# Kernel tuning notes

Measured on AMD Instinct MI355X. Metric: run time of the kernel, lower is better.

The kernel has to match this reference:

```python
import jax, jax.numpy as jnp
import numpy as np

B, SQ, SKV, D = 4, 4096, 4096, 64

def setup_inputs() -> dict:
    key = jax.random.key(0)
    kq, kk, kv = jax.random.split(key, 3)
    return {
        "q": jax.random.normal(kq, (B, SQ, D), dtype=jnp.float32),
        "k": jax.random.normal(kk, (B, SKV, D), dtype=jnp.float32),
        "v": jax.random.normal(kv, (B, SKV, D), dtype=jnp.float32),
        "inv_scale_factor": 8,
        "is_training": 0,
    }

def reference(q, k, v, inv_scale_factor, is_training):
    # qk = q @ k^T, divided by inv_scale_factor, softmax over keys
    scores = jnp.einsum("bqd,bkd->bqk", q, k) / inv_scale_factor  # [B,SQ,SKV]
    attn = jax.nn.softmax(scores, axis=-1)
    # dropout is deterministic identity (eval mode, is_training=0)
    out = jnp.einsum("bqk,bkd->bqd", attn, v)  # [B,SQ,D]
    # should_apply_residual before loop
    out = out + q
    # 3-iteration chain: residual add + normalization add (+2q), dropout (identity),
    # sigmoid, clamp(0,1)
    for _ in range(3):
        out = out + 2.0 * q
        out = jax.nn.sigmoid(out)
        out = jnp.clip(out, 0.0, 1.0)
    return out
```

## Files before the change

### kernel.cpp

```cpp
#include <hip/hip_runtime.h>

#define SQd 4096
#define SKVd 4096
#define DDIM 64
#define BQ 64
#define BK 32
#define NGROUP 4
#define NTILES (SKVd / BK)
#define TILES_PER_GROUP (NTILES / NGROUP)
#define FRAG_ELEMS 512
#define TILE_ELEMS (4 * FRAG_ELEMS)
#define KWS_ELEMS (4 * NTILES * TILE_ELEMS)

typedef __bf16 bf16x8 __attribute__((ext_vector_type(8)));
typedef __bf16 bf16x2 __attribute__((ext_vector_type(2)));
typedef float floatx4 __attribute__((ext_vector_type(4)));

struct CombS {
    float Ored[BQ][NGROUP][68];
    float Lred[BQ][NGROUP];
};
constexpr size_t SMEM_BYTES = sizeof(CombS);

__global__ __launch_bounds__(256)
void prepack_kernel(const float* __restrict__ k, const float* __restrict__ v,
                    __bf16* __restrict__ ws)
{
    const int t = blockIdx.x * 256 + threadIdx.x;
    const int id   = t & (KWS_ELEMS / 8 - 1);
    const int lane = id & 63;
    const int l16  = lane & 15;
    const int quad = lane >> 4;
    const int h    = (id >> 6) & 3;
    const int tile = (id >> 8) & (NTILES - 1);
    const int b    = id >> 15;
    bf16x8 o;
    if (t < KWS_ELEMS / 8) {
        const int row = tile * BK + (h >> 1) * 16 + l16;
        const int col = (h & 1) * 32 + quad * 8;
        const float* p = k + ((size_t)b * SKVd + row) * DDIM + col;
        const float4 a0 = *(const float4*)p;
        const float4 a1 = *(const float4*)(p + 4);
        o[0] = (__bf16)a0.x; o[1] = (__bf16)a0.y; o[2] = (__bf16)a0.z; o[3] = (__bf16)a0.w;
        o[4] = (__bf16)a1.x; o[5] = (__bf16)a1.y; o[6] = (__bf16)a1.z; o[7] = (__bf16)a1.w;
        ((bf16x8*)ws)[id] = o;
    } else {
        const int col = h * 16 + l16;
        #pragma unroll
        for (int j = 0; j < 8; ++j) {
            const int kk  = quad * 8 + j;
            const int key = tile * BK + (kk >> 1) + 16 * (kk & 1);
            o[j] = (__bf16)v[((size_t)b * SKVd + key) * DDIM + col];
        }
        ((bf16x8*)(ws + KWS_ELEMS))[id] = o;
    }
}

__global__ __launch_bounds__(1024, 4)
void fattn_kernel(const float* __restrict__ q, const int* __restrict__ isf_p,
                  const __bf16* __restrict__ kws, const __bf16* __restrict__ vws,
                  float* __restrict__ out)
{
    __shared__ __align__(16) char smem_raw[SMEM_BYTES];

    const int tid  = threadIdx.x;
    const int wave = tid >> 6;
    const int lane = tid & 63;
    const int l16  = lane & 15;
    const int quad = lane >> 4;
    const int g    = wave >> 2;
    const int wg   = wave & 3;

    __bf16 (*Pw)[40] = (__bf16(*)[40])(smem_raw + wave * 1280);

    const int bidx  = blockIdx.x;
    const int b     = (bidx & 7) >> 1;
    const int qtile = ((bidx & 1) << 5) | (bidx >> 3);

    const float scale = 1.0f / (float)(*isf_p);

    bf16x8 qf[2];
    {
        const int qrow = qtile * BQ + wg * 16 + l16;
        const float* qp = q + ((size_t)b * SQd + qrow) * DDIM + quad * 8;
        #pragma unroll
        for (int hh = 0; hh < 2; ++hh)
            #pragma unroll
            for (int j = 0; j < 8; ++j)
                qf[hh][j] = (__bf16)(qp[hh * 32 + j] * scale);
    }

    const __bf16* kg = kws + ((size_t)b * NTILES + g * TILES_PER_GROUP) * TILE_ELEMS + lane * 8;
    const __bf16* vg = vws + ((size_t)b * NTILES + g * TILES_PER_GROUP) * TILE_ELEMS + lane * 8;

    floatx4 o[4];
    float l_lane[4];
    #pragma unroll
    for (int r = 0; r < 4; ++r) l_lane[r] = 0.0f;
    #pragma unroll
    for (int nb = 0; nb < 4; ++nb)
        #pragma unroll
        for (int r = 0; r < 4; ++r) o[nb][r] = 0.0f;

    const floatx4 zf = {0.0f, 0.0f, 0.0f, 0.0f};

    bf16x8 kf[2][4], vf[2][4];
    #pragma unroll
    for (int h = 0; h < 4; ++h) {
        kf[0][h] = *(const bf16x8*)(kg + h * FRAG_ELEMS);
        vf[0][h] = *(const bf16x8*)(vg + h * FRAG_ELEMS);
    }

    #pragma unroll 2
    for (int it = 0; it < TILES_PER_GROUP; ++it) {
        const int cur = it & 1;
        const int nxt = cur ^ 1;
        const size_t noff = (size_t)(it + 1 < TILES_PER_GROUP ? it + 1 : it) * TILE_ELEMS;
        #pragma unroll
        for (int h = 0; h < 4; ++h) {
            kf[nxt][h] = *(const bf16x8*)(kg + noff + h * FRAG_ELEMS);
            vf[nxt][h] = *(const bf16x8*)(vg + noff + h * FRAG_ELEMS);
        }

        floatx4 s0 = zf, s1 = zf;
        s0 = __builtin_amdgcn_mfma_f32_16x16x32_bf16(qf[0], kf[cur][0], s0, 0, 0, 0);
        s0 = __builtin_amdgcn_mfma_f32_16x16x32_bf16(qf[1], kf[cur][1], s0, 0, 0, 0);
        s1 = __builtin_amdgcn_mfma_f32_16x16x32_bf16(qf[0], kf[cur][2], s1, 0, 0, 0);
        s1 = __builtin_amdgcn_mfma_f32_16x16x32_bf16(qf[1], kf[cur][3], s1, 0, 0, 0);

        #pragma unroll
        for (int r = 0; r < 4; ++r) {
            const float p0 = __expf(s0[r]);
            const float p1 = __expf(s1[r]);
            l_lane[r] += p0 + p1;
            bf16x2 pp;
            pp[0] = (__bf16)p0;
            pp[1] = (__bf16)p1;
            *(bf16x2*)&Pw[quad * 4 + r][2 * l16] = pp;
        }
        const bf16x8 pf = *(const bf16x8*)&Pw[l16][quad * 8];

        #pragma unroll
        for (int nb = 0; nb < 4; ++nb)
            o[nb] = __builtin_amdgcn_mfma_f32_16x16x32_bf16(pf, vf[cur][nb], o[nb], 0, 0, 0);
    }

    #pragma unroll
    for (int r = 0; r < 4; ++r) {
        l_lane[r] += __shfl_xor(l_lane[r], 1);
        l_lane[r] += __shfl_xor(l_lane[r], 2);
        l_lane[r] += __shfl_xor(l_lane[r], 4);
        l_lane[r] += __shfl_xor(l_lane[r], 8);
    }

    __syncthreads();
    CombS& C = *(CombS*)smem_raw;
    #pragma unroll
    for (int nb = 0; nb < 4; ++nb)
        #pragma unroll
        for (int r = 0; r < 4; ++r)
            C.Ored[wg * 16 + quad * 4 + r][g][nb * 16 + l16] = o[nb][r];
    if (l16 == 0) {
        #pragma unroll
        for (int r = 0; r < 4; ++r)
            C.Lred[wg * 16 + quad * 4 + r][g] = l_lane[r];
    }
    __syncthreads();

    {
        const int row = tid >> 4;
        const int d4  = (tid & 15) * 4;
        const float l = C.Lred[row][0] + C.Lred[row][1] + C.Lred[row][2] + C.Lred[row][3];
        float x0 = 0.f, x1 = 0.f, x2 = 0.f, x3 = 0.f;
        #pragma unroll
        for (int gg = 0; gg < NGROUP; ++gg) {
            const float4 og = *(const float4*)&C.Ored[row][gg][d4];
            x0 += og.x; x1 += og.y; x2 += og.z; x3 += og.w;
        }
        const size_t idx = ((size_t)b * SQd + qtile * BQ + row) * DDIM + d4;
        const float4 q4 = *(const float4*)(q + idx);
        const float rl = 1.0f / l;
        float xs[4] = {x0 * rl + q4.x, x1 * rl + q4.y, x2 * rl + q4.z, x3 * rl + q4.w};
        const float qs[4] = {q4.x, q4.y, q4.z, q4.w};
        #pragma unroll
        for (int c = 0; c < 4; ++c) {
            float x = xs[c];
            #pragma unroll
            for (int itc = 0; itc < 3; ++itc) {
                x = x + 2.0f * qs[c];
                x = 1.0f / (1.0f + __expf(-x));
                x = fminf(fmaxf(x, 0.0f), 1.0f);
            }
            xs[c] = x;
        }
        const float4 r4 = {xs[0], xs[1], xs[2], xs[3]};
        *(float4*)(out + idx) = r4;
    }
}

extern "C" void kernel_launch(void* const* d_in, const int* in_sizes, int n_in,
                              void* d_out, int out_size, void* d_ws, size_t ws_size,
                              hipStream_t stream) {
    const float* q = (const float*)d_in[0];
    const float* k = (const float*)d_in[1];
    const float* v = (const float*)d_in[2];
    const int* isf = (const int*)d_in[3];
    float* out = (float*)d_out;
    __bf16* ws = (__bf16*)d_ws;

    prepack_kernel<<<dim3(1024), dim3(256), 0, stream>>>(k, v, ws);

    const int nblocks = 4 * (SQd / BQ);
    fattn_kernel<<<dim3(nblocks), dim3(1024), 0, stream>>>(
        q, isf, ws, ws + KWS_ELEMS, out);
}
```

Baseline: 105.9 us.

## Have each wave cover all 64 query rows and keep P in registers

Each wave now handles all four 16-row query groups against its own slice of the key/value tiles (8 key groups, 512-thread blocks), so every K/V fragment load is reused four times. QK^T is computed transposed (K as the A operand) so the exp'd scores already sit in the MFMA B-operand layout. This removes the per-tile LDS round trip for P, with the V prepack permuted to match. The cost is much higher register pressure (16 output accumulators and 8 Q fragments per wave) and a two-phase LDS reduction across 8 groups.

```diff
diff --git a/kernel.cpp b/kernel.cpp
--- a/kernel.cpp
+++ b/kernel.cpp
@@ -5,22 +5,20 @@
 #define DDIM 64
 #define BQ 64
 #define BK 32
-#define NGROUP 4
+#define NG 8
 #define NTILES (SKVd / BK)
-#define TILES_PER_GROUP (NTILES / NGROUP)
+#define TPG (NTILES / NG)
 #define FRAG_ELEMS 512
 #define TILE_ELEMS (4 * FRAG_ELEMS)
 #define KWS_ELEMS (4 * NTILES * TILE_ELEMS)
 
 typedef __bf16 bf16x8 __attribute__((ext_vector_type(8)));
-typedef __bf16 bf16x2 __attribute__((ext_vector_type(2)));
 typedef float floatx4 __attribute__((ext_vector_type(4)));
 
 struct CombS {
-    float Ored[BQ][NGROUP][68];
-    float Lred[BQ][NGROUP];
+    float Ored[BQ][4][68];
+    float Lred[BQ][NG];
 };
-constexpr size_t SMEM_BYTES = sizeof(CombS);
 
 __global__ __launch_bounds__(256)
 void prepack_kernel(const float* __restrict__ k, const float* __restrict__ v,
@@ -48,30 +46,25 @@
         const int col = h * 16 + l16;
         #pragma unroll
         for (int j = 0; j < 8; ++j) {
-            const int kk  = quad * 8 + j;
-            const int key = tile * BK + (kk >> 1) + 16 * (kk & 1);
+            const int key = tile * BK + 16 * (j >> 2) + quad * 4 + (j & 3);
             o[j] = (__bf16)v[((size_t)b * SKVd + key) * DDIM + col];
         }
         ((bf16x8*)(ws + KWS_ELEMS))[id] = o;
     }
 }
 
-__global__ __launch_bounds__(1024, 4)
+__global__ __launch_bounds__(512, 2)
 void fattn_kernel(const float* __restrict__ q, const int* __restrict__ isf_p,
                   const __bf16* __restrict__ kws, const __bf16* __restrict__ vws,
                   float* __restrict__ out)
 {
-    __shared__ __align__(16) char smem_raw[SMEM_BYTES];
+    __shared__ __align__(16) CombS C;
 
     const int tid  = threadIdx.x;
-    const int wave = tid >> 6;
+    const int g    = tid >> 6;
     const int lane = tid & 63;
     const int l16  = lane & 15;
     const int quad = lane >> 4;
-    const int g    = wave >> 2;
-    const int wg   = wave & 3;
-
-    __bf16 (*Pw)[40] = (__bf16(*)[40])(smem_raw + wave * 1280);
 
     const int bidx  = blockIdx.x;
     const int b     = (bidx & 7) >> 1;
@@ -79,122 +72,149 @@
 
     const float scale = 1.0f / (float)(*isf_p);
 
-    bf16x8 qf[2];
+    bf16x8 qf[4][2];
+    #pragma unroll
+    for (int qg = 0; qg < 4; ++qg) {
+        const int qrow = qtile * BQ + qg * 16 + l16;
+        const float* qp = q + ((size_t)b * SQd + qrow) * DDIM + quad * 8;
+        #pragma unroll
+        for (int dh = 0; dh < 2; ++dh) {
+            const float4 a0 = *(const float4*)(qp + dh * 32);
+            const float4 a1 = *(const float4*)(qp + dh * 32 + 4);
+            qf[qg][dh][0] = (__bf16)(a0.x * scale); qf[qg][dh][1] = (__bf16)(a0.y * scale);
+            qf[qg][dh][2] = (__bf16)(a0.z * scale); qf[qg][dh][3] = (__bf16)(a0.w * scale);
+            qf[qg][dh][4] = (__bf16)(a1.x * scale); qf[qg][dh][5] = (__bf16)(a1.y * scale);
+            qf[qg][dh][6] = (__bf16)(a1.z * scale); qf[qg][dh][7] = (__bf16)(a1.w * scale);
+        }
+    }
+
+    const __bf16* kg = kws + ((size_t)b * NTILES + g * TPG) * TILE_ELEMS + lane * 8;
+    const __bf16* vg = vws + ((size_t)b * NTILES + g * TPG) * TILE_ELEMS + lane * 8;
+
+    floatx4 o[4][4];
+    float l_acc[4];
+    #pragma unroll
+    for (int qg = 0; qg < 4; ++qg) {
+        l_acc[qg] = 0.0f;
+        #pragma unroll
+        for (int nb = 0; nb < 4; ++nb)
+            #pragma unroll
+            for (int r = 0; r < 4; ++r) o[qg][nb][r] = 0.0f;
+    }
+
+    const floatx4 zf = {0.0f, 0.0f, 0.0f, 0.0f};
+
+    auto step = [&](bf16x8* kc, bf16x8* vc, bf16x8* kn, bf16x8* vn, int itn) {
+        const size_t noff = (size_t)itn * TILE_ELEMS;
+        #pragma unroll
+        for (int h = 0; h < 4; ++h)
+            kn[h] = *(const bf16x8*)(kg + noff + h * FRAG_ELEMS);
+        #pragma unroll
+        for (int h = 0; h < 4; ++h)
+            vn[h] = *(const bf16x8*)(vg + noff + h * FRAG_ELEMS);
+
+        bf16x8 pf[4];
+        #pragma unroll
+        for (int qg = 0; qg < 4; ++qg) {
+            floatx4 s0 = zf, s1 = zf;
+            s0 = __builtin_amdgcn_mfma_f32_16x16x32_bf16(kc[0], qf[qg][0], s0, 0, 0, 0);
+            s0 = __builtin_amdgcn_mfma_f32_16x16x32_bf16(kc[1], qf[qg][1], s0, 0, 0, 0);
+            s1 = __builtin_amdgcn_mfma_f32_16x16x32_bf16(kc[2], qf[qg][0], s1, 0, 0, 0);
+            s1 = __builtin_amdgcn_mfma_f32_16x16x32_bf16(kc[3], qf[qg][1], s1, 0, 0, 0);
+            float lsum = 0.0f;
+            #pragma unroll
+            for (int r = 0; r < 4; ++r) {
+                const float p0 = __expf(s0[r]);
+                const float p1 = __expf(s1[r]);
+                pf[qg][r]     = (__bf16)p0;
+                pf[qg][4 + r] = (__bf16)p1;
+                lsum += p0 + p1;
+            }
+            l_acc[qg] += lsum;
+        }
+        #pragma unroll
+        for (int nb = 0; nb < 4; ++nb)
+            #pragma unroll
+            for (int qg = 0; qg < 4; ++qg)
+                o[qg][nb] = __builtin_amdgcn_mfma_f32_16x16x32_bf16(pf[qg], vc[nb], o[qg][nb], 0, 0, 0);
+    };
+
+    bf16x8 k0[4], v0[4], k1[4], v1[4];
+    #pragma unroll
+    for (int h = 0; h < 4; ++h) {
+        k0[h] = *(const bf16x8*)(kg + h * FRAG_ELEMS);
+        v0[h] = *(const bf16x8*)(vg + h * FRAG_ELEMS);
+    }
+    for (int t = 0; t < TPG / 2; ++t) {
+        step(k0, v0, k1, v1, 2 * t + 1);
+        step(k1, v1, k0, v0, (2 * t + 2 < TPG) ? 2 * t + 2 : TPG - 1);
+    }
+
+    #pragma unroll
+    for (int qg = 0; qg < 4; ++qg) {
+        l_acc[qg] += __shfl_xor(l_acc[qg], 16);
+        l_acc[qg] += __shfl_xor(l_acc[qg], 32);
+    }
+    if (quad == 0) {
+        #pragma unroll
+        for (int qg = 0; qg < 4; ++qg)
+            C.Lred[qg * 16 + l16][g] = l_acc[qg];
+    }
+
+    if (g < 4) {
+        #pragma unroll
+        for (int qg = 0; qg < 4; ++qg)
+            #pragma unroll
+            for (int nb = 0; nb < 4; ++nb)
+                #pragma unroll
+                for (int r = 0; r < 4; ++r)
+                    C.Ored[qg * 16 + quad * 4 + r][g][nb * 16 + l16] = o[qg][nb][r];
+    }
+    __syncthreads();
+    if (g >= 4) {
+        #pragma unroll
+        for (int qg = 0; qg < 4; ++qg)
+            #pragma unroll
+            for (int nb = 0; nb < 4; ++nb)
+                #pragma unroll
+                for (int r = 0; r < 4; ++r)
+                    C.Ored[qg * 16 + quad * 4 + r][g - 4][nb * 16 + l16] += o[qg][nb][r];
+    }
+    __syncthreads();
+
     {
-        const int qrow = qtile * BQ + wg * 16 + l16;
-        const float* qp = q + ((size_t)b * SQd + qrow) * DDIM + quad * 8;
-        #pragma unroll
-        for (int hh = 0; hh < 2; ++hh)
-            #pragma unroll
-            for (int j = 0; j < 8; ++j)
-                qf[hh][j] = (__bf16)(qp[hh * 32 + j] * scale);
-    }
-
-    const __bf16* kg = kws + ((size_t)b * NTILES + g * TILES_PER_GROUP) * TILE_ELEMS + lane * 8;
-    const __bf16* vg = vws + ((size_t)b * NTILES + g * TILES_PER_GROUP) * TILE_ELEMS + lane * 8;
-
-    floatx4 o[4];
-    float l_lane[4];
-    #pragma unroll
-    for (int r = 0; r < 4; ++r) l_lane[r] = 0.0f;
-    #pragma unroll
-    for (int nb = 0; nb < 4; ++nb)
-        #pragma unroll
-        for (int r = 0; r < 4; ++r) o[nb][r] = 0.0f;
-
-    const floatx4 zf = {0.0f, 0.0f, 0.0f, 0.0f};
-
-    bf16x8 kf[2][4], vf[2][4];
-    #pragma unroll
-    for (int h = 0; h < 4; ++h) {
-        kf[0][h] = *(const bf16x8*)(kg + h * FRAG_ELEMS);
-        vf[0][h] = *(const bf16x8*)(vg + h * FRAG_ELEMS);
-    }
-
-    #pragma unroll 2
-    for (int it = 0; it < TILES_PER_GROUP; ++it) {
-        const int cur = it & 1;
-        const int nxt = cur ^ 1;
-        const size_t noff = (size_t)(it + 1 < TILES_PER_GROUP ? it + 1 : it) * TILE_ELEMS;
-        #pragma unroll
-        for (int h = 0; h < 4; ++h) {
-            kf[nxt][h] = *(const bf16x8*)(kg + noff + h * FRAG_ELEMS);
-            vf[nxt][h] = *(const bf16x8*)(vg + noff + h * FRAG_ELEMS);
-        }
-
-        floatx4 s0 = zf, s1 = zf;
-        s0 = __builtin_amdgcn_mfma_f32_16x16x32_bf16(qf[0], kf[cur][0], s0, 0, 0, 0);
-        s0 = __builtin_amdgcn_mfma_f32_16x16x32_bf16(qf[1], kf[cur][1], s0, 0, 0, 0);
-        s1 = __builtin_amdgcn_mfma_f32_16x16x32_bf16(qf[0], kf[cur][2], s1, 0, 0, 0);
-        s1 = __builtin_amdgcn_mfma_f32_16x16x32_bf16(qf[1], kf[cur][3], s1, 0, 0, 0);
-
-        #pragma unroll
-        for (int r = 0; r < 4; ++r) {
-            const float p0 = __expf(s0[r]);
-            const float p1 = __expf(s1[r]);
-            l_lane[r] += p0 + p1;
-            bf16x2 pp;
-            pp[0] = (__bf16)p0;
-            pp[1] = (__bf16)p1;
-            *(bf16x2*)&Pw[quad * 4 + r][2 * l16] = pp;
-        }
-        const bf16x8 pf = *(const bf16x8*)&Pw[l16][quad * 8];
-
-        #pragma unroll
-        for (int nb = 0; nb < 4; ++nb)
-            o[nb] = __builtin_amdgcn_mfma_f32_16x16x32_bf16(pf, vf[cur][nb], o[nb], 0, 0, 0);
-    }
-
-    #pragma unroll
-    for (int r = 0; r < 4; ++r) {
-        l_lane[r] += __shfl_xor(l_lane[r], 1);
-        l_lane[r] += __shfl_xor(l_lane[r], 2);
-        l_lane[r] += __shfl_xor(l_lane[r], 4);
-        l_lane[r] += __shfl_xor(l_lane[r], 8);
-    }
-
-    __syncthreads();
-    CombS& C = *(CombS*)smem_raw;
-    #pragma unroll
-    for (int nb = 0; nb < 4; ++nb)
-        #pragma unroll
-        for (int r = 0; r < 4; ++r)
-            C.Ored[wg * 16 + quad * 4 + r][g][nb * 16 + l16] = o[nb][r];
-    if (l16 == 0) {
-        #pragma unroll
-        for (int r = 0; r < 4; ++r)
-            C.Lred[wg * 16 + quad * 4 + r][g] = l_lane[r];
-    }
-    __syncthreads();
-
-    {
-        const int row = tid >> 4;
-        const int d4  = (tid & 15) * 4;
-        const float l = C.Lred[row][0] + C.Lred[row][1] + C.Lred[row][2] + C.Lred[row][3];
-        float x0 = 0.f, x1 = 0.f, x2 = 0.f, x3 = 0.f;
-        #pragma unroll
-        for (int gg = 0; gg < NGROUP; ++gg) {
-            const float4 og = *(const float4*)&C.Ored[row][gg][d4];
-            x0 += og.x; x1 += og.y; x2 += og.z; x3 += og.w;
-        }
-        const size_t idx = ((size_t)b * SQd + qtile * BQ + row) * DDIM + d4;
-        const float4 q4 = *(const float4*)(q + idx);
+        const int row = tid >> 3;
+        const int d8  = (tid & 7) * 8;
+        float l = 0.0f;
+        #pragma unroll
+        for (int gg = 0; gg < NG; ++gg) l += C.Lred[row][gg];
         const float rl = 1.0f / l;
-        float xs[4] = {x0 * rl + q4.x, x1 * rl + q4.y, x2 * rl + q4.z, x3 * rl + q4.w};
-        const float qs[4] = {q4.x, q4.y, q4.z, q4.w};
-        #pragma unroll
-        for (int c = 0; c < 4; ++c) {
-            float x = xs[c];
-            #pragma unroll
-            for (int itc = 0; itc < 3; ++itc) {
-                x = x + 2.0f * qs[c];
-                x = 1.0f / (1.0f + __expf(-x));
-                x = fminf(fmaxf(x, 0.0f), 1.0f);
+        #pragma unroll
+        for (int half = 0; half < 2; ++half) {
+            const int d4 = d8 + half * 4;
+            float xs[4] = {0.f, 0.f, 0.f, 0.f};
+            #pragma unroll
+            for (int s = 0; s < 4; ++s) {
+                const float4 t4 = *(const float4*)&C.Ored[row][s][d4];
+                xs[0] += t4.x; xs[1] += t4.y; xs[2] += t4.z; xs[3] += t4.w;
             }
-            xs[c] = x;
-        }
-        const float4 r4 = {xs[0], xs[1], xs[2], xs[3]};
-        *(float4*)(out + idx) = r4;
+            const size_t idx = ((size_t)b * SQd + qtile * BQ + row) * DDIM + d4;
+            const float4 q4 = *(const float4*)(q + idx);
+            const float qs[4] = {q4.x, q4.y, q4.z, q4.w};
+            #pragma unroll
+            for (int c = 0; c < 4; ++c) {
+                float x = xs[c] * rl + qs[c];
+                #pragma unroll
+                for (int itc = 0; itc < 3; ++itc) {
+                    x = x + 2.0f * qs[c];
+                    x = 1.0f / (1.0f + __expf(-x));
+                    x = fminf(fmaxf(x, 0.0f), 1.0f);
+                }
+                xs[c] = x;
+            }
+            const float4 r4 = {xs[0], xs[1], xs[2], xs[3]};
+            *(float4*)(out + idx) = r4;
+        }
     }
 }
 
@@ -211,6 +231,6 @@
     prepack_kernel<<<dim3(1024), dim3(256), 0, stream>>>(k, v, ws);
 
     const int nblocks = 4 * (SQd / BQ);
-    fattn_kernel<<<dim3(nblocks), dim3(1024), 0, stream>>>(
+    fattn_kernel<<<dim3(nblocks), dim3(512), 0, stream>>>(
         q, isf, ws, ws + KWS_ELEMS, out);
 }
```

Measured after the change: 92.63 us. 12.6% less time.
